# Optimization experiments

Hardware: AMD Instinct MI355X
Metric: run time of the kernel (lower is better)

The kernel has to match this reference:

```python
import jax, jax.numpy as jnp
import numpy as np

# ---- static configuration (mirrors scalar_python args) ----
N_SHOTS = 8
NZ = NX = 300
FD_PAD = 2                 # accuracy 4 -> fd_pad = accuracy // 2
NZP = NZ + 2 * FD_PAD      # 304
NXP = NX + 2 * FD_PAD      # 304
NT = 50
N_SRC = 1
N_REC = 300
DT = 0.001
DX = 4.0
INV_DX = 1.0 / DX
INV_DX2 = 1.0 / (DX * DX)
FLAT = NZP * NXP


def _shift(x, axis, s):
    """result[i] = x[i + s] along `axis`, zero-filled outside (matches padded-grid stencil)."""
    n = x.shape[axis]
    pad = [(0, 0)] * x.ndim
    if s > 0:
        xs = jax.lax.slice_in_dim(x, s, n, axis=axis)
        pad[axis] = (0, s)
    else:
        xs = jax.lax.slice_in_dim(x, 0, n + s, axis=axis)
        pad[axis] = (-s, 0)
    return jnp.pad(xs, pad)


def diff1(x, axis):
    """4th-order accurate central first derivative * (1/dx)."""
    return ((_shift(x, axis, 1) - _shift(x, axis, -1)) * (2.0 / 3.0)
            + (_shift(x, axis, -2) - _shift(x, axis, 2)) * (1.0 / 12.0)) * INV_DX


def diff2(x, axis):
    """4th-order accurate central second derivative * (1/dx^2)."""
    return ((-2.5) * x
            + (4.0 / 3.0) * (_shift(x, axis, 1) + _shift(x, axis, -1))
            - (1.0 / 12.0) * (_shift(x, axis, 2) + _shift(x, axis, -2))) * INV_DX2


def _forward_step(v2dt2, wfc, wfp, psi, zeta, a, b, dbdx):
    """One FDTD time step with PML (faithful to deepwave _forward_step, ndim=2)."""
    new_psi, new_zeta = [], []
    w_sum = jnp.zeros_like(wfc)
    for dim in range(2):          # dim 0 = z (axis 1), dim 1 = x (axis 2)
        axis = dim + 1
        dudx = diff1(wfc, axis)
        tmp = ((1.0 + b[dim]) * diff2(wfc, axis)
               + dbdx[dim] * dudx
               + diff1(a[dim] * psi[dim], axis))
        w_sum = w_sum + (1.0 + b[dim]) * tmp + a[dim] * zeta[dim]
        new_psi.append(b[dim] * dudx + a[dim] * psi[dim])
        new_zeta.append(b[dim] * tmp + a[dim] * zeta[dim])
    wfc_new = v2dt2 * w_sum + 2.0 * wfc - wfp
    return wfc_new, new_psi, new_zeta


def setup_inputs() -> dict:
    key = jax.random.key(0)
    ks = jax.random.split(key, 10)
    v = 1500.0 + 1000.0 * jax.random.uniform(ks[0], (NZP, NXP), jnp.float32)
    source_amplitudes = jax.random.normal(ks[1], (NT, N_SHOTS, N_SRC), jnp.float32)
    # PML profiles: (a, b, dbdx) per spatial dim, broadcastable 1D profiles.
    a_z = -0.1 * jax.random.uniform(ks[2], (NZP, 1), jnp.float32)
    b_z = 0.1 * jax.random.uniform(ks[3], (NZP, 1), jnp.float32)
    dbdx_z = 0.01 * jax.random.normal(ks[4], (NZP, 1), jnp.float32)
    a_x = -0.1 * jax.random.uniform(ks[5], (1, NXP), jnp.float32)
    b_x = 0.1 * jax.random.uniform(ks[6], (1, NXP), jnp.float32)
    dbdx_x = 0.01 * jax.random.normal(ks[7], (1, NXP), jnp.float32)
    sources_i = jax.random.randint(ks[8], (N_SHOTS, N_SRC), 0, FLAT, jnp.int32)
    receivers_i = jax.random.randint(ks[9], (N_SHOTS, N_REC), 0, FLAT, jnp.int32)
    return {"v": v, "source_amplitudes": source_amplitudes,
            "a_z": a_z, "b_z": b_z, "dbdx_z": dbdx_z,
            "a_x": a_x, "b_x": b_x, "dbdx_x": dbdx_x,
            "sources_i": sources_i, "receivers_i": receivers_i}


def reference(v, source_amplitudes, a_z, b_z, dbdx_z, a_x, b_x, dbdx_x,
              sources_i, receivers_i):
    v2dt2 = (v * v) * (DT * DT)                 # (NZP, NXP), broadcasts over shots
    a = (a_z, a_x)
    b = (b_z, b_x)
    dbdx = (dbdx_z, dbdx_x)
    shot_idx = jnp.arange(N_SHOTS)[:, None]
    zeros = jnp.zeros((N_SHOTS, NZP, NXP), v.dtype)

    def body(carry, amp_t):
        wfc, wfp, pz, px, zz, zx = carry
        # record receivers from the current wavefield (before the step)
        rec = jnp.take_along_axis(wfc.reshape(N_SHOTS, -1), receivers_i, axis=1)
        wfc_new, (pzn, pxn), (zzn, zxn) = _forward_step(
            v2dt2, wfc, wfp, (pz, px), (zz, zx), a, b, dbdx)
        # inject sources into the new wavefield (scatter-add of flat indices)
        flat = wfc_new.reshape(N_SHOTS, -1).at[shot_idx, sources_i].add(amp_t)
        wfc_new = flat.reshape(N_SHOTS, NZP, NXP)
        return (wfc_new, wfc, pzn, pxn, zzn, zxn), rec

    init = (zeros, zeros, zeros, zeros, zeros, zeros)
    _, receiver_amplitudes = jax.lax.scan(body, init, source_amplitudes)
    return receiver_amplitudes   # (NT, N_SHOTS, N_REC)
```

## Files before the change

kernel.cpp:

```cpp
#include <hip/hip_runtime.h>

#define N_SHOTS 8
#define NZP 304
#define NXP 304
#define NT 50
#define N_REC 300
#define FLAT (NZP * NXP)
#define DT 0.001f
#define INV_DX 0.25f
#define INV_DX2 0.0625f

#define C23 (2.0f / 3.0f)
#define C112 (1.0f / 12.0f)
#define C43 (4.0f / 3.0f)

union F4 { float4 v; float f[4]; };

__device__ __forceinline__ F4 ldf4(const float* p) {
    F4 r; r.v = *reinterpret_cast<const float4*>(p); return r;
}
__device__ __forceinline__ F4 zf4() {
    F4 r; r.v = make_float4(0.f, 0.f, 0.f, 0.f); return r;
}

__global__ __launch_bounds__(320) void fdtd_step4(
    const float* __restrict__ v,
    const float* __restrict__ amp,
    const float* __restrict__ az, const float* __restrict__ bz, const float* __restrict__ dbz,
    const float* __restrict__ ax, const float* __restrict__ bx, const float* __restrict__ dbx,
    const int* __restrict__ src_i,
    const int* __restrict__ rec_i,
    const float* __restrict__ wc,
    float* __restrict__ wp,
    const float* __restrict__ pzi, float* __restrict__ pzo,
    const float* __restrict__ pxi, float* __restrict__ pxo,
    float* __restrict__ zz, float* __restrict__ zx,
    float* __restrict__ rec_out,
    int t)
{
    const int bid = blockIdx.x;
    const int shot = bid & 7;
    const int jg = bid >> 3;
    const int tid = threadIdx.x;

    if (tid >= 304) {
        if (jg < 19) {
            int ridx = jg * 16 + (tid - 304);
            if (ridx < N_REC) {
                rec_out[t * (N_SHOTS * N_REC) + shot * N_REC + ridx] =
                    wc[shot * FLAT + rec_i[shot * N_REC + ridx]];
            }
        }
        return;
    }

    const int r = tid / 76;
    const int i = tid - r * 76;
    const int z = jg * 4 + r;
    const int x0 = 4 * i;
    const int idx = shot * FLAT + z * NXP + x0;

    const bool lok = (i > 0), rok = (i < 75);
    F4 wCx = ldf4(wc + idx);
    F4 wLx = lok ? ldf4(wc + idx - 4) : zf4();
    F4 wRx = rok ? ldf4(wc + idx + 4) : zf4();
    F4 pCx = ldf4(pxi + idx);
    F4 pLx = lok ? ldf4(pxi + idx - 4) : zf4();
    F4 pRx = rok ? ldf4(pxi + idx + 4) : zf4();
    F4 aCx = ldf4(ax + x0);
    F4 aLx = lok ? ldf4(ax + x0 - 4) : zf4();
    F4 aRx = rok ? ldf4(ax + x0 + 4) : zf4();

    float wx[12], apx[12];
    #pragma unroll
    for (int k = 0; k < 4; ++k) {
        wx[k]     = wLx.f[k];  apx[k]     = aLx.f[k] * pLx.f[k];
        wx[4 + k] = wCx.f[k];  apx[4 + k] = aCx.f[k] * pCx.f[k];
        wx[8 + k] = wRx.f[k];  apx[8 + k] = aRx.f[k] * pRx.f[k];
    }

    const bool m1 = (z >= 1), m2 = (z >= 2), p1 = (z < NZP - 1), p2 = (z < NZP - 2);
    F4 wzm1 = m1 ? ldf4(wc + idx - NXP)     : zf4();
    F4 wzm2 = m2 ? ldf4(wc + idx - 2 * NXP) : zf4();
    F4 wzp1 = p1 ? ldf4(wc + idx + NXP)     : zf4();
    F4 wzp2 = p2 ? ldf4(wc + idx + 2 * NXP) : zf4();
    const float azm1 = m1 ? az[z - 1] : 0.f;
    const float azm2 = m2 ? az[z - 2] : 0.f;
    const float azp1 = p1 ? az[z + 1] : 0.f;
    const float azp2 = p2 ? az[z + 2] : 0.f;
    F4 qzm1 = m1 ? ldf4(pzi + idx - NXP)     : zf4();
    F4 qzm2 = m2 ? ldf4(pzi + idx - 2 * NXP) : zf4();
    F4 qzp1 = p1 ? ldf4(pzi + idx + NXP)     : zf4();
    F4 qzp2 = p2 ? ldf4(pzi + idx + 2 * NXP) : zf4();
    #pragma unroll
    for (int k = 0; k < 4; ++k) {
        qzm1.f[k] *= azm1; qzm2.f[k] *= azm2;
        qzp1.f[k] *= azp1; qzp2.f[k] *= azp2;
    }

    F4 pzC = ldf4(pzi + idx);
    F4 zzC = ldf4(zz + idx);
    F4 zxC = ldf4(zx + idx);
    F4 vC  = ldf4(v + z * NXP + x0);
    F4 wpC = ldf4(wp + idx);
    F4 bxC = ldf4(bx + x0);
    F4 dxC = ldf4(dbx + x0);
    const float azc = az[z], bzc = bz[z], dbzc = dbz[z];
    const int srci = src_i[shot];
    const float amp_t = amp[t * N_SHOTS + shot];

    F4 o_w, o_pz, o_px, o_zz, o_zx;

    #pragma unroll
    for (int k = 0; k < 4; ++k) {
        const float c = wx[4 + k];
        const float d1x  = ((wx[5 + k] - wx[3 + k]) * C23 + (wx[2 + k] - wx[6 + k]) * C112) * INV_DX;
        const float d2x  = (-2.5f * c + C43 * (wx[5 + k] + wx[3 + k]) - C112 * (wx[6 + k] + wx[2 + k])) * INV_DX2;
        const float dapx = ((apx[5 + k] - apx[3 + k]) * C23 + (apx[2 + k] - apx[6 + k]) * C112) * INV_DX;
        const float d1z  = ((wzp1.f[k] - wzm1.f[k]) * C23 + (wzm2.f[k] - wzp2.f[k]) * C112) * INV_DX;
        const float d2z  = (-2.5f * c + C43 * (wzp1.f[k] + wzm1.f[k]) - C112 * (wzp2.f[k] + wzm2.f[k])) * INV_DX2;
        const float dapz = ((qzp1.f[k] - qzm1.f[k]) * C23 + (qzm2.f[k] - qzp2.f[k]) * C112) * INV_DX;

        const float tmpz = (1.f + bzc) * d2z + dbzc * d1z + dapz;
        float w_sum = (1.f + bzc) * tmpz + azc * zzC.f[k];

        const float bxk = bxC.f[k], axk = aCx.f[k];
        const float tmpx = (1.f + bxk) * d2x + dxC.f[k] * d1x + dapx;
        w_sum += (1.f + bxk) * tmpx + axk * zxC.f[k];

        const float vv = vC.f[k];
        float wn = (vv * vv) * (DT * DT) * w_sum + 2.f * c - wpC.f[k];
        if (z * NXP + x0 + k == srci) wn += amp_t;

        o_w.f[k]  = wn;
        o_pz.f[k] = bzc * d1z + azc * pzC.f[k];
        o_px.f[k] = bxk * d1x + apx[4 + k];
        o_zz.f[k] = bzc * tmpz + azc * zzC.f[k];
        o_zx.f[k] = bxk * tmpx + axk * zxC.f[k];
    }

    *reinterpret_cast<float4*>(wp + idx)  = o_w.v;
    *reinterpret_cast<float4*>(pzo + idx) = o_pz.v;
    *reinterpret_cast<float4*>(pxo + idx) = o_px.v;
    *reinterpret_cast<float4*>(zz + idx)  = o_zz.v;
    *reinterpret_cast<float4*>(zx + idx)  = o_zx.v;
}

extern "C" void kernel_launch(void* const* d_in, const int* in_sizes, int n_in,
                              void* d_out, int out_size, void* d_ws, size_t ws_size,
                              hipStream_t stream) {
    const float* v     = (const float*)d_in[0];
    const float* amp   = (const float*)d_in[1];
    const float* az    = (const float*)d_in[2];
    const float* bz    = (const float*)d_in[3];
    const float* dbz   = (const float*)d_in[4];
    const float* ax    = (const float*)d_in[5];
    const float* bx    = (const float*)d_in[6];
    const float* dbx   = (const float*)d_in[7];
    const int* src_i   = (const int*)d_in[8];
    const int* rec_i   = (const int*)d_in[9];
    float* out = (float*)d_out;

    float* ws = (float*)d_ws;
    const size_t A = (size_t)N_SHOTS * FLAT;

    float* wf0 = ws + 0 * A; float* wf1 = ws + 1 * A;
    float* pz0 = ws + 2 * A; float* px0 = ws + 3 * A;
    float* zz  = ws + 4 * A; float* zx  = ws + 5 * A;
    float* pz1 = ws + 6 * A; float* px1 = ws + 7 * A;

    hipMemsetAsync(d_ws, 0, 6 * A * sizeof(float), stream);

    float* wf[2] = { wf0, wf1 };
    float* pz[2] = { pz0, pz1 };
    float* px[2] = { px0, px1 };

    int cur = 0;
    for (int t = 0; t < NT; ++t) {
        fdtd_step4<<<8 * 76, 320, 0, stream>>>(
            v, amp, az, bz, dbz, ax, bx, dbx, src_i, rec_i,
            wf[cur], wf[1 - cur],
            pz[cur], pz[1 - cur],
            px[cur], px[1 - cur],
            zz, zx, out, t);
        cur ^= 1;
    }
}
```

Before: 434.1 us.

## Fuse two FDTD time steps per launch with shared-memory halo recompute

Each block computes one time step over an 8-row tile plus 2-row halos into LDS. It then computes the next step from LDS, writing only the second step's fields to global memory. Receivers for the intermediate step are read from LDS. This halves kernel launches and global round-trips of the intermediate fields. In exchange it recomputes halo rows, needs about 63 KB of LDS, which limits occupancy, and doubles the workspace buffer count.

```diff
diff --git a/kernel.cpp b/kernel.cpp
--- a/kernel.cpp
+++ b/kernel.cpp
@@ -14,8 +14,10 @@
 #define C112 (1.0f / 12.0f)
 #define C43 (4.0f / 3.0f)
 
+#define RR 8
+#define AR 12
+
 union F4 { float4 v; float f[4]; };
-
 __device__ __forceinline__ F4 ldf4(const float* p) {
     F4 r; r.v = *reinterpret_cast<const float4*>(p); return r;
 }
@@ -23,7 +25,7 @@
     F4 r; r.v = make_float4(0.f, 0.f, 0.f, 0.f); return r;
 }
 
-__global__ __launch_bounds__(320) void fdtd_step4(
+__global__ __launch_bounds__(320) void fdtd_step2(
     const float* __restrict__ v,
     const float* __restrict__ amp,
     const float* __restrict__ az, const float* __restrict__ bz, const float* __restrict__ dbz,
@@ -31,119 +33,229 @@
     const int* __restrict__ src_i,
     const int* __restrict__ rec_i,
     const float* __restrict__ wc,
-    float* __restrict__ wp,
+    const float* __restrict__ wp,
+    float* __restrict__ w1g,
+    float* __restrict__ w2g,
     const float* __restrict__ pzi, float* __restrict__ pzo,
     const float* __restrict__ pxi, float* __restrict__ pxo,
-    float* __restrict__ zz, float* __restrict__ zx,
+    const float* __restrict__ zzi, float* __restrict__ zzo,
+    const float* __restrict__ zxi, float* __restrict__ zxo,
     float* __restrict__ rec_out,
     int t)
 {
+    __shared__ float w1s[AR][NXP];
+    __shared__ float qzs[AR][NXP];
+    __shared__ float qxs[RR][NXP];
+    __shared__ float azzs[RR][NXP];
+    __shared__ float azxs[RR][NXP];
+
     const int bid = blockIdx.x;
     const int shot = bid & 7;
-    const int jg = bid >> 3;
+    const int g = bid >> 3;
     const int tid = threadIdx.x;
+    const int z0 = g * RR;
+    const int srci = src_i[shot];
+    const int sbase = shot * FLAT;
 
     if (tid >= 304) {
-        if (jg < 19) {
-            int ridx = jg * 16 + (tid - 304);
-            if (ridx < N_REC) {
+        if (g < 19) {
+            int ridx = g * 16 + (tid - 304);
+            if (ridx < N_REC)
                 rec_out[t * (N_SHOTS * N_REC) + shot * N_REC + ridx] =
-                    wc[shot * FLAT + rec_i[shot * N_REC + ridx]];
-            }
+                    wc[sbase + rec_i[shot * N_REC + ridx]];
         }
-        return;
+    } else {
+        const float ampA = amp[t * N_SHOTS + shot];
+        const int r4 = tid / 76;
+        const int i = tid - r4 * 76;
+        const int x0 = 4 * i;
+        const bool lok = (i > 0), rok = (i < 75);
+
+        for (int ra = 0; ra < 3; ++ra) {
+            const int la = r4 + 4 * ra;
+            const int zA = z0 - 2 + la;
+            if (zA < 0 || zA >= NZP) {
+                *reinterpret_cast<float4*>(&w1s[la][x0]) = make_float4(0,0,0,0);
+                *reinterpret_cast<float4*>(&qzs[la][x0]) = make_float4(0,0,0,0);
+                continue;
+            }
+            const int idx = sbase + zA * NXP + x0;
+
+            F4 wCx = ldf4(wc + idx);
+            F4 wLx = lok ? ldf4(wc + idx - 4) : zf4();
+            F4 wRx = rok ? ldf4(wc + idx + 4) : zf4();
+            F4 pCx = ldf4(pxi + idx);
+            F4 pLx = lok ? ldf4(pxi + idx - 4) : zf4();
+            F4 pRx = rok ? ldf4(pxi + idx + 4) : zf4();
+            F4 aCx = ldf4(ax + x0);
+            F4 aLx = lok ? ldf4(ax + x0 - 4) : zf4();
+            F4 aRx = rok ? ldf4(ax + x0 + 4) : zf4();
+            float wxw[12], apx[12];
+            #pragma unroll
+            for (int k = 0; k < 4; ++k) {
+                wxw[k]     = wLx.f[k];  apx[k]     = aLx.f[k] * pLx.f[k];
+                wxw[4 + k] = wCx.f[k];  apx[4 + k] = aCx.f[k] * pCx.f[k];
+                wxw[8 + k] = wRx.f[k];  apx[8 + k] = aRx.f[k] * pRx.f[k];
+            }
+
+            const bool m1 = (zA >= 1), m2 = (zA >= 2), p1 = (zA < NZP - 1), p2 = (zA < NZP - 2);
+            F4 wzm1 = m1 ? ldf4(wc + idx - NXP)     : zf4();
+            F4 wzm2 = m2 ? ldf4(wc + idx - 2 * NXP) : zf4();
+            F4 wzp1 = p1 ? ldf4(wc + idx + NXP)     : zf4();
+            F4 wzp2 = p2 ? ldf4(wc + idx + 2 * NXP) : zf4();
+            const float azm1 = m1 ? az[zA - 1] : 0.f;
+            const float azm2 = m2 ? az[zA - 2] : 0.f;
+            const float azp1 = p1 ? az[zA + 1] : 0.f;
+            const float azp2 = p2 ? az[zA + 2] : 0.f;
+            F4 qzm1 = m1 ? ldf4(pzi + idx - NXP)     : zf4();
+            F4 qzm2 = m2 ? ldf4(pzi + idx - 2 * NXP) : zf4();
+            F4 qzp1 = p1 ? ldf4(pzi + idx + NXP)     : zf4();
+            F4 qzp2 = p2 ? ldf4(pzi + idx + 2 * NXP) : zf4();
+            #pragma unroll
+            for (int k = 0; k < 4; ++k) {
+                qzm1.f[k] *= azm1; qzm2.f[k] *= azm2;
+                qzp1.f[k] *= azp1; qzp2.f[k] *= azp2;
+            }
+
+            F4 pzC = ldf4(pzi + idx);
+            F4 zzC = ldf4(zzi + idx);
+            F4 zxC = ldf4(zxi + idx);
+            F4 vC  = ldf4(v + zA * NXP + x0);
+            F4 wpC = ldf4(wp + idx);
+            F4 bxC = ldf4(bx + x0);
+            F4 dxC = ldf4(dbx + x0);
+            const float azc = az[zA], bzc = bz[zA], dbzc = dbz[zA];
+
+            F4 o_w1, o_qz, o_qx, o_azz, o_azx;
+            #pragma unroll
+            for (int k = 0; k < 4; ++k) {
+                const float c = wxw[4 + k];
+                const float d1x  = ((wxw[5+k] - wxw[3+k]) * C23 + (wxw[2+k] - wxw[6+k]) * C112) * INV_DX;
+                const float d2x  = (-2.5f * c + C43 * (wxw[5+k] + wxw[3+k]) - C112 * (wxw[6+k] + wxw[2+k])) * INV_DX2;
+                const float dapx = ((apx[5+k] - apx[3+k]) * C23 + (apx[2+k] - apx[6+k]) * C112) * INV_DX;
+                const float d1z  = ((wzp1.f[k] - wzm1.f[k]) * C23 + (wzm2.f[k] - wzp2.f[k]) * C112) * INV_DX;
+                const float d2z  = (-2.5f * c + C43 * (wzp1.f[k] + wzm1.f[k]) - C112 * (wzp2.f[k] + wzm2.f[k])) * INV_DX2;
+                const float dapz = ((qzp1.f[k] - qzm1.f[k]) * C23 + (qzm2.f[k] - qzp2.f[k]) * C112) * INV_DX;
+
+                const float tmpz = (1.f + bzc) * d2z + dbzc * d1z + dapz;
+                float w_sum = (1.f + bzc) * tmpz + azc * zzC.f[k];
+                const float bxk = bxC.f[k], axk = aCx.f[k];
+                const float tmpx = (1.f + bxk) * d2x + dxC.f[k] * d1x + dapx;
+                w_sum += (1.f + bxk) * tmpx + axk * zxC.f[k];
+
+                const float vv = vC.f[k];
+                float wn = (vv * vv) * (DT * DT) * w_sum + 2.f * c - wpC.f[k];
+                if (zA * NXP + x0 + k == srci) wn += ampA;
+
+                o_w1.f[k]  = wn;
+                const float psiz = bzc * d1z + azc * pzC.f[k];
+                o_qz.f[k]  = azc * psiz;
+                const float psix = bxk * d1x + apx[4 + k];
+                o_qx.f[k]  = axk * psix;
+                const float ztz  = bzc * tmpz + azc * zzC.f[k];
+                o_azz.f[k] = azc * ztz;
+                const float ztx  = bxk * tmpx + axk * zxC.f[k];
+                o_azx.f[k] = axk * ztx;
+            }
+            *reinterpret_cast<float4*>(&w1s[la][x0]) = o_w1.v;
+            *reinterpret_cast<float4*>(&qzs[la][x0]) = o_qz.v;
+            if (la >= 2 && la < 10) {
+                *reinterpret_cast<float4*>(&qxs[la - 2][x0])  = o_qx.v;
+                *reinterpret_cast<float4*>(&azzs[la - 2][x0]) = o_azz.v;
+                *reinterpret_cast<float4*>(&azxs[la - 2][x0]) = o_azx.v;
+                *reinterpret_cast<float4*>(w1g + idx) = o_w1.v;
+            }
+        }
     }
 
-    const int r = tid / 76;
-    const int i = tid - r * 76;
-    const int z = jg * 4 + r;
-    const int x0 = 4 * i;
-    const int idx = shot * FLAT + z * NXP + x0;
-
-    const bool lok = (i > 0), rok = (i < 75);
-    F4 wCx = ldf4(wc + idx);
-    F4 wLx = lok ? ldf4(wc + idx - 4) : zf4();
-    F4 wRx = rok ? ldf4(wc + idx + 4) : zf4();
-    F4 pCx = ldf4(pxi + idx);
-    F4 pLx = lok ? ldf4(pxi + idx - 4) : zf4();
-    F4 pRx = rok ? ldf4(pxi + idx + 4) : zf4();
-    F4 aCx = ldf4(ax + x0);
-    F4 aLx = lok ? ldf4(ax + x0 - 4) : zf4();
-    F4 aRx = rok ? ldf4(ax + x0 + 4) : zf4();
-
-    float wx[12], apx[12];
-    #pragma unroll
-    for (int k = 0; k < 4; ++k) {
-        wx[k]     = wLx.f[k];  apx[k]     = aLx.f[k] * pLx.f[k];
-        wx[4 + k] = wCx.f[k];  apx[4 + k] = aCx.f[k] * pCx.f[k];
-        wx[8 + k] = wRx.f[k];  apx[8 + k] = aRx.f[k] * pRx.f[k];
+    __syncthreads();
+
+    if (tid < 304) {
+        const float ampB = amp[(t + 1) * N_SHOTS + shot];
+        const int r4 = tid / 76;
+        const int i = tid - r4 * 76;
+        const int x0 = 4 * i;
+        const bool lok = (i > 0), rok = (i < 75);
+
+        for (int rb = 0; rb < 2; ++rb) {
+            const int lo = r4 + 4 * rb;
+            const int la = lo + 2;
+            const int z = z0 + lo;
+            const int idx = sbase + z * NXP + x0;
+
+            F4 wC = ldf4(&w1s[la][x0]);
+            F4 wL = lok ? ldf4(&w1s[la][x0 - 4]) : zf4();
+            F4 wR = rok ? ldf4(&w1s[la][x0 + 4]) : zf4();
+            F4 qC = ldf4(&qxs[lo][x0]);
+            F4 qL = lok ? ldf4(&qxs[lo][x0 - 4]) : zf4();
+            F4 qR = rok ? ldf4(&qxs[lo][x0 + 4]) : zf4();
+            float wxw[12], apx[12];
+            #pragma unroll
+            for (int k = 0; k < 4; ++k) {
+                wxw[k]     = wL.f[k];  apx[k]     = qL.f[k];
+                wxw[4 + k] = wC.f[k];  apx[4 + k] = qC.f[k];
+                wxw[8 + k] = wR.f[k];  apx[8 + k] = qR.f[k];
+            }
+            F4 wzm1 = ldf4(&w1s[la - 1][x0]);
+            F4 wzm2 = ldf4(&w1s[la - 2][x0]);
+            F4 wzp1 = ldf4(&w1s[la + 1][x0]);
+            F4 wzp2 = ldf4(&w1s[la + 2][x0]);
+            F4 qzm1 = ldf4(&qzs[la - 1][x0]);
+            F4 qzm2 = ldf4(&qzs[la - 2][x0]);
+            F4 qzp1 = ldf4(&qzs[la + 1][x0]);
+            F4 qzp2 = ldf4(&qzs[la + 2][x0]);
+            F4 qzC  = ldf4(&qzs[la][x0]);
+            F4 azzC = ldf4(&azzs[lo][x0]);
+            F4 azxC = ldf4(&azxs[lo][x0]);
+            F4 vC   = ldf4(v + z * NXP + x0);
+            F4 wold = ldf4(wc + idx);
+            F4 bxC  = ldf4(bx + x0);
+            F4 dxC  = ldf4(dbx + x0);
+            const float azc = az[z], bzc = bz[z], dbzc = dbz[z];
+
+            F4 o_w2, o_pz, o_px, o_zz, o_zx;
+            #pragma unroll
+            for (int k = 0; k < 4; ++k) {
+                const float c = wxw[4 + k];
+                const float d1x  = ((wxw[5+k] - wxw[3+k]) * C23 + (wxw[2+k] - wxw[6+k]) * C112) * INV_DX;
+                const float d2x  = (-2.5f * c + C43 * (wxw[5+k] + wxw[3+k]) - C112 * (wxw[6+k] + wxw[2+k])) * INV_DX2;
+                const float dapx = ((apx[5+k] - apx[3+k]) * C23 + (apx[2+k] - apx[6+k]) * C112) * INV_DX;
+                const float d1z  = ((wzp1.f[k] - wzm1.f[k]) * C23 + (wzm2.f[k] - wzp2.f[k]) * C112) * INV_DX;
+                const float d2z  = (-2.5f * c + C43 * (wzp1.f[k] + wzm1.f[k]) - C112 * (wzp2.f[k] + wzm2.f[k])) * INV_DX2;
+                const float dapz = ((qzp1.f[k] - qzm1.f[k]) * C23 + (qzm2.f[k] - qzp2.f[k]) * C112) * INV_DX;
+
+                const float tmpz = (1.f + bzc) * d2z + dbzc * d1z + dapz;
+                float w_sum = (1.f + bzc) * tmpz + azzC.f[k];
+                const float bxk = bxC.f[k];
+                const float tmpx = (1.f + bxk) * d2x + dxC.f[k] * d1x + dapx;
+                w_sum += (1.f + bxk) * tmpx + azxC.f[k];
+
+                const float vv = vC.f[k];
+                float wn = (vv * vv) * (DT * DT) * w_sum + 2.f * c - wold.f[k];
+                if (z * NXP + x0 + k == srci) wn += ampB;
+
+                o_w2.f[k] = wn;
+                o_pz.f[k] = bzc * d1z + qzC.f[k];
+                o_px.f[k] = bxk * d1x + qC.f[k];
+                o_zz.f[k] = bzc * tmpz + azzC.f[k];
+                o_zx.f[k] = bxk * tmpx + azxC.f[k];
+            }
+            *reinterpret_cast<float4*>(w2g + idx) = o_w2.v;
+            *reinterpret_cast<float4*>(pzo + idx) = o_pz.v;
+            *reinterpret_cast<float4*>(pxo + idx) = o_px.v;
+            *reinterpret_cast<float4*>(zzo + idx) = o_zz.v;
+            *reinterpret_cast<float4*>(zxo + idx) = o_zx.v;
+        }
     }
 
-    const bool m1 = (z >= 1), m2 = (z >= 2), p1 = (z < NZP - 1), p2 = (z < NZP - 2);
-    F4 wzm1 = m1 ? ldf4(wc + idx - NXP)     : zf4();
-    F4 wzm2 = m2 ? ldf4(wc + idx - 2 * NXP) : zf4();
-    F4 wzp1 = p1 ? ldf4(wc + idx + NXP)     : zf4();
-    F4 wzp2 = p2 ? ldf4(wc + idx + 2 * NXP) : zf4();
-    const float azm1 = m1 ? az[z - 1] : 0.f;
-    const float azm2 = m2 ? az[z - 2] : 0.f;
-    const float azp1 = p1 ? az[z + 1] : 0.f;
-    const float azp2 = p2 ? az[z + 2] : 0.f;
-    F4 qzm1 = m1 ? ldf4(pzi + idx - NXP)     : zf4();
-    F4 qzm2 = m2 ? ldf4(pzi + idx - 2 * NXP) : zf4();
-    F4 qzp1 = p1 ? ldf4(pzi + idx + NXP)     : zf4();
-    F4 qzp2 = p2 ? ldf4(pzi + idx + 2 * NXP) : zf4();
-    #pragma unroll
-    for (int k = 0; k < 4; ++k) {
-        qzm1.f[k] *= azm1; qzm2.f[k] *= azm2;
-        qzp1.f[k] *= azp1; qzp2.f[k] *= azp2;
+    if (tid < N_REC) {
+        const int rc = rec_i[shot * N_REC + tid];
+        const int rz = rc / NXP;
+        if (rz >= z0 && rz < z0 + RR) {
+            rec_out[(t + 1) * (N_SHOTS * N_REC) + shot * N_REC + tid] =
+                w1s[rz - z0 + 2][rc - rz * NXP];
+        }
     }
-
-    F4 pzC = ldf4(pzi + idx);
-    F4 zzC = ldf4(zz + idx);
-    F4 zxC = ldf4(zx + idx);
-    F4 vC  = ldf4(v + z * NXP + x0);
-    F4 wpC = ldf4(wp + idx);
-    F4 bxC = ldf4(bx + x0);
-    F4 dxC = ldf4(dbx + x0);
-    const float azc = az[z], bzc = bz[z], dbzc = dbz[z];
-    const int srci = src_i[shot];
-    const float amp_t = amp[t * N_SHOTS + shot];
-
-    F4 o_w, o_pz, o_px, o_zz, o_zx;
-
-    #pragma unroll
-    for (int k = 0; k < 4; ++k) {
-        const float c = wx[4 + k];
-        const float d1x  = ((wx[5 + k] - wx[3 + k]) * C23 + (wx[2 + k] - wx[6 + k]) * C112) * INV_DX;
-        const float d2x  = (-2.5f * c + C43 * (wx[5 + k] + wx[3 + k]) - C112 * (wx[6 + k] + wx[2 + k])) * INV_DX2;
-        const float dapx = ((apx[5 + k] - apx[3 + k]) * C23 + (apx[2 + k] - apx[6 + k]) * C112) * INV_DX;
-        const float d1z  = ((wzp1.f[k] - wzm1.f[k]) * C23 + (wzm2.f[k] - wzp2.f[k]) * C112) * INV_DX;
-        const float d2z  = (-2.5f * c + C43 * (wzp1.f[k] + wzm1.f[k]) - C112 * (wzp2.f[k] + wzm2.f[k])) * INV_DX2;
-        const float dapz = ((qzp1.f[k] - qzm1.f[k]) * C23 + (qzm2.f[k] - qzp2.f[k]) * C112) * INV_DX;
-
-        const float tmpz = (1.f + bzc) * d2z + dbzc * d1z + dapz;
-        float w_sum = (1.f + bzc) * tmpz + azc * zzC.f[k];
-
-        const float bxk = bxC.f[k], axk = aCx.f[k];
-        const float tmpx = (1.f + bxk) * d2x + dxC.f[k] * d1x + dapx;
-        w_sum += (1.f + bxk) * tmpx + axk * zxC.f[k];
-
-        const float vv = vC.f[k];
-        float wn = (vv * vv) * (DT * DT) * w_sum + 2.f * c - wpC.f[k];
-        if (z * NXP + x0 + k == srci) wn += amp_t;
-
-        o_w.f[k]  = wn;
-        o_pz.f[k] = bzc * d1z + azc * pzC.f[k];
-        o_px.f[k] = bxk * d1x + apx[4 + k];
-        o_zz.f[k] = bzc * tmpz + azc * zzC.f[k];
-        o_zx.f[k] = bxk * tmpx + axk * zxC.f[k];
-    }
-
-    *reinterpret_cast<float4*>(wp + idx)  = o_w.v;
-    *reinterpret_cast<float4*>(pzo + idx) = o_pz.v;
-    *reinterpret_cast<float4*>(pxo + idx) = o_px.v;
-    *reinterpret_cast<float4*>(zz + idx)  = o_zz.v;
-    *reinterpret_cast<float4*>(zx + idx)  = o_zx.v;
 }
 
 extern "C" void kernel_launch(void* const* d_in, const int* in_sizes, int n_in,
@@ -164,25 +276,29 @@
     float* ws = (float*)d_ws;
     const size_t A = (size_t)N_SHOTS * FLAT;
 
-    float* wf0 = ws + 0 * A; float* wf1 = ws + 1 * A;
-    float* pz0 = ws + 2 * A; float* px0 = ws + 3 * A;
-    float* zz  = ws + 4 * A; float* zx  = ws + 5 * A;
-    float* pz1 = ws + 6 * A; float* px1 = ws + 7 * A;
+    float* X   = ws + 0 * A;
+    float* Y   = ws + 1 * A;
+    float* PZI = ws + 2 * A;   float* PXI = ws + 3 * A;
+    float* ZZI = ws + 4 * A;   float* ZXI = ws + 5 * A;
+    float* Z   = ws + 6 * A;
+    float* W   = ws + 7 * A;
+    float* PZO = ws + 8 * A;   float* PXO = ws + 9 * A;
+    float* ZZO = ws + 10 * A;  float* ZXO = ws + 11 * A;
 
     hipMemsetAsync(d_ws, 0, 6 * A * sizeof(float), stream);
 
-    float* wf[2] = { wf0, wf1 };
-    float* pz[2] = { pz0, pz1 };
-    float* px[2] = { px0, px1 };
-
-    int cur = 0;
-    for (int t = 0; t < NT; ++t) {
-        fdtd_step4<<<8 * 76, 320, 0, stream>>>(
+    for (int k = 0; k < NT / 2; ++k) {
+        fdtd_step2<<<N_SHOTS * (NZP / RR), 320, 0, stream>>>(
             v, amp, az, bz, dbz, ax, bx, dbx, src_i, rec_i,
-            wf[cur], wf[1 - cur],
-            pz[cur], pz[1 - cur],
-            px[cur], px[1 - cur],
-            zz, zx, out, t);
-        cur ^= 1;
+            X, Y, Z, W,
+            PZI, PZO, PXI, PXO, ZZI, ZZO, ZXI, ZXO,
+            out, 2 * k);
+        float* oX = X; float* oY = Y;
+        X = W; Y = Z; Z = oX; W = oY;
+        float* tp;
+        tp = PZI; PZI = PZO; PZO = tp;
+        tp = PXI; PXI = PXO; PXO = tp;
+        tp = ZZI; ZZI = ZZO; ZZO = tp;
+        tp = ZXI; ZXI = ZXO; ZXO = tp;
     }
 }
```

Result: slower. 516.2 us (+18.9%).

## Remap work to 512 blocks with 361 float4 chunks per block

Applied to the files above, without the earlier changes.

The grid goes from 608 blocks (4 rows each) to 512 blocks, each covering a contiguous run of 361 float4 chunks per shot. Threads loop up to twice, so the 304 grid rows are split evenly into 64 chunk groups per shot. The likely aim is to match the block count to the CU count (256 CUs, two blocks each) and avoid a partial second wave. In exchange only part of each block's threads do a second pass, which gives lane imbalance and more work per thread.

```diff
diff --git a/kernel.cpp b/kernel.cpp
--- a/kernel.cpp
+++ b/kernel.cpp
@@ -14,8 +14,9 @@
 #define C112 (1.0f / 12.0f)
 #define C43 (4.0f / 3.0f)
 
+#define NCH 361
+
 union F4 { float4 v; float f[4]; };
-
 __device__ __forceinline__ F4 ldf4(const float* p) {
     F4 r; r.v = *reinterpret_cast<const float4*>(p); return r;
 }
@@ -40,110 +41,118 @@
 {
     const int bid = blockIdx.x;
     const int shot = bid & 7;
-    const int jg = bid >> 3;
+    const int j = bid >> 3;
     const int tid = threadIdx.x;
+    const int sbase = shot * FLAT;
 
-    if (tid >= 304) {
-        if (jg < 19) {
-            int ridx = jg * 16 + (tid - 304);
+    if (tid >= NXP) {
+        if (j < 19) {
+            int ridx = j * 16 + (tid - NXP);
             if (ridx < N_REC) {
                 rec_out[t * (N_SHOTS * N_REC) + shot * N_REC + ridx] =
-                    wc[shot * FLAT + rec_i[shot * N_REC + ridx]];
+                    wc[sbase + rec_i[shot * N_REC + ridx]];
             }
         }
         return;
     }
 
-    const int r = tid / 76;
-    const int i = tid - r * 76;
-    const int z = jg * 4 + r;
-    const int x0 = 4 * i;
-    const int idx = shot * FLAT + z * NXP + x0;
-
-    const bool lok = (i > 0), rok = (i < 75);
-    F4 wCx = ldf4(wc + idx);
-    F4 wLx = lok ? ldf4(wc + idx - 4) : zf4();
-    F4 wRx = rok ? ldf4(wc + idx + 4) : zf4();
-    F4 pCx = ldf4(pxi + idx);
-    F4 pLx = lok ? ldf4(pxi + idx - 4) : zf4();
-    F4 pRx = rok ? ldf4(pxi + idx + 4) : zf4();
-    F4 aCx = ldf4(ax + x0);
-    F4 aLx = lok ? ldf4(ax + x0 - 4) : zf4();
-    F4 aRx = rok ? ldf4(ax + x0 + 4) : zf4();
-
-    float wx[12], apx[12];
-    #pragma unroll
-    for (int k = 0; k < 4; ++k) {
-        wx[k]     = wLx.f[k];  apx[k]     = aLx.f[k] * pLx.f[k];
-        wx[4 + k] = wCx.f[k];  apx[4 + k] = aCx.f[k] * pCx.f[k];
-        wx[8 + k] = wRx.f[k];  apx[8 + k] = aRx.f[k] * pRx.f[k];
-    }
-
-    const bool m1 = (z >= 1), m2 = (z >= 2), p1 = (z < NZP - 1), p2 = (z < NZP - 2);
-    F4 wzm1 = m1 ? ldf4(wc + idx - NXP)     : zf4();
-    F4 wzm2 = m2 ? ldf4(wc + idx - 2 * NXP) : zf4();
-    F4 wzp1 = p1 ? ldf4(wc + idx + NXP)     : zf4();
-    F4 wzp2 = p2 ? ldf4(wc + idx + 2 * NXP) : zf4();
-    const float azm1 = m1 ? az[z - 1] : 0.f;
-    const float azm2 = m2 ? az[z - 2] : 0.f;
-    const float azp1 = p1 ? az[z + 1] : 0.f;
-    const float azp2 = p2 ? az[z + 2] : 0.f;
-    F4 qzm1 = m1 ? ldf4(pzi + idx - NXP)     : zf4();
-    F4 qzm2 = m2 ? ldf4(pzi + idx - 2 * NXP) : zf4();
-    F4 qzp1 = p1 ? ldf4(pzi + idx + NXP)     : zf4();
-    F4 qzp2 = p2 ? ldf4(pzi + idx + 2 * NXP) : zf4();
-    #pragma unroll
-    for (int k = 0; k < 4; ++k) {
-        qzm1.f[k] *= azm1; qzm2.f[k] *= azm2;
-        qzp1.f[k] *= azp1; qzp2.f[k] *= azp2;
-    }
-
-    F4 pzC = ldf4(pzi + idx);
-    F4 zzC = ldf4(zz + idx);
-    F4 zxC = ldf4(zx + idx);
-    F4 vC  = ldf4(v + z * NXP + x0);
-    F4 wpC = ldf4(wp + idx);
-    F4 bxC = ldf4(bx + x0);
-    F4 dxC = ldf4(dbx + x0);
-    const float azc = az[z], bzc = bz[z], dbzc = dbz[z];
     const int srci = src_i[shot];
     const float amp_t = amp[t * N_SHOTS + shot];
-
-    F4 o_w, o_pz, o_px, o_zz, o_zx;
+    const int chbase = j * NCH;
 
     #pragma unroll
-    for (int k = 0; k < 4; ++k) {
-        const float c = wx[4 + k];
-        const float d1x  = ((wx[5 + k] - wx[3 + k]) * C23 + (wx[2 + k] - wx[6 + k]) * C112) * INV_DX;
-        const float d2x  = (-2.5f * c + C43 * (wx[5 + k] + wx[3 + k]) - C112 * (wx[6 + k] + wx[2 + k])) * INV_DX2;
-        const float dapx = ((apx[5 + k] - apx[3 + k]) * C23 + (apx[2 + k] - apx[6 + k]) * C112) * INV_DX;
-        const float d1z  = ((wzp1.f[k] - wzm1.f[k]) * C23 + (wzm2.f[k] - wzp2.f[k]) * C112) * INV_DX;
-        const float d2z  = (-2.5f * c + C43 * (wzp1.f[k] + wzm1.f[k]) - C112 * (wzp2.f[k] + wzm2.f[k])) * INV_DX2;
-        const float dapz = ((qzp1.f[k] - qzm1.f[k]) * C23 + (qzm2.f[k] - qzp2.f[k]) * C112) * INV_DX;
+    for (int p = 0; p < 2; ++p) {
+        const int chl = tid + 304 * p;
+        if (p == 1 && tid >= NCH - 304) break;
+        const int ch = chbase + chl;
+        const int z = ch / 76;
+        const int i = ch - z * 76;
+        const int x0 = 4 * i;
+        const int idx = sbase + 4 * ch;
 
-        const float tmpz = (1.f + bzc) * d2z + dbzc * d1z + dapz;
-        float w_sum = (1.f + bzc) * tmpz + azc * zzC.f[k];
+        const bool lok = (i > 0), rok = (i < 75);
+        F4 wCx = ldf4(wc + idx);
+        F4 wLx = lok ? ldf4(wc + idx - 4) : zf4();
+        F4 wRx = rok ? ldf4(wc + idx + 4) : zf4();
+        F4 pCx = ldf4(pxi + idx);
+        F4 pLx = lok ? ldf4(pxi + idx - 4) : zf4();
+        F4 pRx = rok ? ldf4(pxi + idx + 4) : zf4();
+        F4 aCx = ldf4(ax + x0);
+        F4 aLx = lok ? ldf4(ax + x0 - 4) : zf4();
+        F4 aRx = rok ? ldf4(ax + x0 + 4) : zf4();
 
-        const float bxk = bxC.f[k], axk = aCx.f[k];
-        const float tmpx = (1.f + bxk) * d2x + dxC.f[k] * d1x + dapx;
-        w_sum += (1.f + bxk) * tmpx + axk * zxC.f[k];
+        float wx[12], apx[12];
+        #pragma unroll
+        for (int k = 0; k < 4; ++k) {
+            wx[k]     = wLx.f[k];  apx[k]     = aLx.f[k] * pLx.f[k];
+            wx[4 + k] = wCx.f[k];  apx[4 + k] = aCx.f[k] * pCx.f[k];
+            wx[8 + k] = wRx.f[k];  apx[8 + k] = aRx.f[k] * pRx.f[k];
+        }
 
-        const float vv = vC.f[k];
-        float wn = (vv * vv) * (DT * DT) * w_sum + 2.f * c - wpC.f[k];
-        if (z * NXP + x0 + k == srci) wn += amp_t;
+        const bool m1 = (z >= 1), m2 = (z >= 2), p1 = (z < NZP - 1), p2 = (z < NZP - 2);
+        F4 wzm1 = m1 ? ldf4(wc + idx - NXP)     : zf4();
+        F4 wzm2 = m2 ? ldf4(wc + idx - 2 * NXP) : zf4();
+        F4 wzp1 = p1 ? ldf4(wc + idx + NXP)     : zf4();
+        F4 wzp2 = p2 ? ldf4(wc + idx + 2 * NXP) : zf4();
+        const float azm1 = m1 ? az[z - 1] : 0.f;
+        const float azm2 = m2 ? az[z - 2] : 0.f;
+        const float azp1 = p1 ? az[z + 1] : 0.f;
+        const float azp2 = p2 ? az[z + 2] : 0.f;
+        F4 qzm1 = m1 ? ldf4(pzi + idx - NXP)     : zf4();
+        F4 qzm2 = m2 ? ldf4(pzi + idx - 2 * NXP) : zf4();
+        F4 qzp1 = p1 ? ldf4(pzi + idx + NXP)     : zf4();
+        F4 qzp2 = p2 ? ldf4(pzi + idx + 2 * NXP) : zf4();
+        #pragma unroll
+        for (int k = 0; k < 4; ++k) {
+            qzm1.f[k] *= azm1; qzm2.f[k] *= azm2;
+            qzp1.f[k] *= azp1; qzp2.f[k] *= azp2;
+        }
 
-        o_w.f[k]  = wn;
-        o_pz.f[k] = bzc * d1z + azc * pzC.f[k];
-        o_px.f[k] = bxk * d1x + apx[4 + k];
-        o_zz.f[k] = bzc * tmpz + azc * zzC.f[k];
-        o_zx.f[k] = bxk * tmpx + axk * zxC.f[k];
+        F4 pzC = ldf4(pzi + idx);
+        F4 zzC = ldf4(zz + idx);
+        F4 zxC = ldf4(zx + idx);
+        F4 vC  = ldf4(v + 4 * ch);
+        F4 wpC = ldf4(wp + idx);
+        F4 bxC = ldf4(bx + x0);
+        F4 dxC = ldf4(dbx + x0);
+        const float azc = az[z], bzc = bz[z], dbzc = dbz[z];
+
+        F4 o_w, o_pz, o_px, o_zz, o_zx;
+
+        #pragma unroll
+        for (int k = 0; k < 4; ++k) {
+            const float c = wx[4 + k];
+            const float d1x  = ((wx[5 + k] - wx[3 + k]) * C23 + (wx[2 + k] - wx[6 + k]) * C112) * INV_DX;
+            const float d2x  = (-2.5f * c + C43 * (wx[5 + k] + wx[3 + k]) - C112 * (wx[6 + k] + wx[2 + k])) * INV_DX2;
+            const float dapx = ((apx[5 + k] - apx[3 + k]) * C23 + (apx[2 + k] - apx[6 + k]) * C112) * INV_DX;
+            const float d1z  = ((wzp1.f[k] - wzm1.f[k]) * C23 + (wzm2.f[k] - wzp2.f[k]) * C112) * INV_DX;
+            const float d2z  = (-2.5f * c + C43 * (wzp1.f[k] + wzm1.f[k]) - C112 * (wzp2.f[k] + wzm2.f[k])) * INV_DX2;
+            const float dapz = ((qzp1.f[k] - qzm1.f[k]) * C23 + (qzm2.f[k] - qzp2.f[k]) * C112) * INV_DX;
+
+            const float tmpz = (1.f + bzc) * d2z + dbzc * d1z + dapz;
+            float w_sum = (1.f + bzc) * tmpz + azc * zzC.f[k];
+
+            const float bxk = bxC.f[k], axk = aCx.f[k];
+            const float tmpx = (1.f + bxk) * d2x + dxC.f[k] * d1x + dapx;
+            w_sum += (1.f + bxk) * tmpx + axk * zxC.f[k];
+
+            const float vv = vC.f[k];
+            float wn = (vv * vv) * (DT * DT) * w_sum + 2.f * c - wpC.f[k];
+            if (4 * ch + k == srci) wn += amp_t;
+
+            o_w.f[k]  = wn;
+            o_pz.f[k] = bzc * d1z + azc * pzC.f[k];
+            o_px.f[k] = bxk * d1x + apx[4 + k];
+            o_zz.f[k] = bzc * tmpz + azc * zzC.f[k];
+            o_zx.f[k] = bxk * tmpx + axk * zxC.f[k];
+        }
+
+        *reinterpret_cast<float4*>(wp + idx)  = o_w.v;
+        *reinterpret_cast<float4*>(pzo + idx) = o_pz.v;
+        *reinterpret_cast<float4*>(pxo + idx) = o_px.v;
+        *reinterpret_cast<float4*>(zz + idx)  = o_zz.v;
+        *reinterpret_cast<float4*>(zx + idx)  = o_zx.v;
     }
-
-    *reinterpret_cast<float4*>(wp + idx)  = o_w.v;
-    *reinterpret_cast<float4*>(pzo + idx) = o_pz.v;
-    *reinterpret_cast<float4*>(pxo + idx) = o_px.v;
-    *reinterpret_cast<float4*>(zz + idx)  = o_zz.v;
-    *reinterpret_cast<float4*>(zx + idx)  = o_zx.v;
 }
 
 extern "C" void kernel_launch(void* const* d_in, const int* in_sizes, int n_in,
@@ -177,7 +186,7 @@
 
     int cur = 0;
     for (int t = 0; t < NT; ++t) {
-        fdtd_step4<<<8 * 76, 320, 0, stream>>>(
+        fdtd_step4<<<512, 320, 0, stream>>>(
             v, amp, az, bz, dbz, ax, bx, dbx, src_i, rec_i,
             wf[cur], wf[1 - cur],
             pz[cur], pz[1 - cur],
```

Measured after the change: 415.3 us. -4.3%, faster.
